# Kernel tuning notes

Measured on AMD Instinct MI355X. Metric: run time of the kernel, lower is better.

## Reference

```python
import jax, jax.numpy as jnp
import numpy as np

N, E = 25000, 400000
ATOM, INV, DNODE, DEDGE = 64, 64, 128, 128
HID = 6 * INV  # invariance_net hidden = 4*inv + 2*inv


def _shift(x):
    # out[:-1] = x[1:]; out[-1] = 0  (matches torch zeros_like + slice assign)
    return jnp.concatenate([x[1:], jnp.zeros_like(x[:1])], axis=0)


def _ln(x, g, b):
    m = jnp.mean(x, axis=-1, keepdims=True)
    v = jnp.var(x, axis=-1, keepdims=True)
    return (x - m) * jax.lax.rsqrt(v + 1e-6) * g + b


def _block(x, w1, b1, g, bb, w2, b2):
    # Linear -> LayerNorm -> SiLU -> Linear
    h = jax.nn.silu(_ln(x @ w1.T + b1, g, bb))
    return h @ w2.T + b2


def _linear_params(key, din, dout):
    k1, k2 = jax.random.split(key)
    lim = 1.0 / np.sqrt(din)
    w = jax.random.uniform(k1, (dout, din), minval=-lim, maxval=lim, dtype=jnp.float32)
    b = jax.random.uniform(k2, (dout,), minval=-lim, maxval=lim, dtype=jnp.float32)
    return w, b


def setup_inputs():
    key = jax.random.key(0)
    ks = jax.random.split(key, 12)
    atom_embedded = jax.random.normal(ks[0], (N, ATOM), jnp.float32)
    edge_length_embedded = jax.random.normal(ks[1], (E, INV), jnp.float32)
    edge_vec = jax.random.normal(ks[2], (E, 3), jnp.float32)
    src = jnp.sort(jax.random.randint(ks[3], (E,), 0, N))  # neighbor-list layout
    dst = jax.random.randint(ks[4], (E,), 0, N)
    edge_index = jnp.stack([src, dst])
    aw1, ab1 = _linear_params(ks[5], 1, INV)
    aw2, ab2 = _linear_params(ks[6], INV, INV)
    iw1, ib1 = _linear_params(ks[7], 3 * INV + 3 * ATOM, HID)
    iw2, ib2 = _linear_params(ks[8], HID, DNODE)
    mw1, mb1 = _linear_params(ks[9], 2 * DNODE + INV, 2 * INV)
    mw2, mb2 = _linear_params(ks[10], 2 * INV, DEDGE)
    return dict(
        atom_embedded=atom_embedded, edge_length_embedded=edge_length_embedded,
        edge_vec=edge_vec, edge_index=edge_index,
        angle_w1=aw1, angle_b1=ab1, angle_g=jnp.ones(INV), angle_bn=jnp.zeros(INV),
        angle_w2=aw2, angle_b2=ab2,
        inv_w1=iw1, inv_b1=ib1, inv_g=jnp.ones(HID), inv_bn=jnp.zeros(HID),
        inv_w2=iw2, inv_b2=ib2,
        mrg_w1=mw1, mrg_b1=mb1, mrg_g=jnp.ones(2 * INV), mrg_bn=jnp.zeros(2 * INV),
        mrg_w2=mw2, mrg_b2=mb2,
    )


def _forward(atom_embedded, edge_length_embedded, edge_vec, edge_index,
             angle_w1, angle_b1, angle_g, angle_bn, angle_w2, angle_b2,
             inv_w1, inv_b1, inv_g, inv_bn, inv_w2, inv_b2,
             mrg_w1, mrg_b1, mrg_g, mrg_bn, mrg_w2, mrg_b2):
    src, dst = edge_index[0], edge_index[1]
    src_s, dst_s = _shift(src), _shift(dst)
    mask = (src == src_s) & (src != dst) & (src_s != dst_s)
    e = src.shape[0]
    ar = jnp.arange(e)
    # torch does nonzero(mask)[:-1]: drop the LAST true index from the mask
    last = jnp.max(jnp.where(mask, ar, -1))
    mask = mask & (ar != last)
    vn = edge_vec / jnp.linalg.norm(edge_vec, axis=-1, keepdims=True)
    vn = jnp.where(mask[:, None], vn, 0.0)  # edge_vec_norm (zeros off-mask)
    cos = jnp.sum(vn * _shift(vn), axis=-1, keepdims=True)  # [E,1]
    ang = _block(cos, angle_w1, angle_b1, angle_g, angle_bn, angle_w2, angle_b2)
    el_s = _shift(edge_length_embedded)
    feat = jnp.concatenate([atom_embedded[src], atom_embedded[dst], edge_length_embedded,
                            atom_embedded[dst_s], el_s, ang], axis=-1)  # [E, 3*INV+3*ATOM]
    feat = jnp.where(mask[:, None], feat, 0.0)
    node_msg = _block(feat, inv_w1, inv_b1, inv_g, inv_bn, inv_w2, inv_b2)  # [E, DNODE]
    node = jax.ops.segment_sum(node_msg, dst, num_segments=atom_embedded.shape[0])
    edge = _block(jnp.concatenate([node[src], node[dst], edge_length_embedded], axis=-1),
                  mrg_w1, mrg_b1, mrg_g, mrg_bn, mrg_w2, mrg_b2)  # [E, DEDGE]
    return node, edge


def reference(atom_embedded, edge_length_embedded, edge_vec, edge_index,
              angle_w1, angle_b1, angle_g, angle_bn, angle_w2, angle_b2,
              inv_w1, inv_b1, inv_g, inv_bn, inv_w2, inv_b2,
              mrg_w1, mrg_b1, mrg_g, mrg_bn, mrg_w2, mrg_b2):
    return _forward(atom_embedded, edge_length_embedded, edge_vec, edge_index,
                    angle_w1, angle_b1, angle_g, angle_bn, angle_w2, angle_b2,
                    inv_w1, inv_b1, inv_g, inv_bn, inv_w2, inv_b2,
                    mrg_w1, mrg_b1, mrg_g, mrg_bn, mrg_w2, mrg_b2)
```

## Files before the change

kernel.cpp:

```cpp
#include <hip/hip_runtime.h>
#include <math.h>


typedef short short8 __attribute__((ext_vector_type(8)));
typedef float f32x4 __attribute__((ext_vector_type(4)));

#define SFA 392
#define SFB 328

__device__ __forceinline__ unsigned short f2bf(float x) {
  union { float f; unsigned u; } v; v.f = x;
  unsigned r = (v.u + 0x7FFFu + ((v.u >> 16) & 1u)) >> 16;
  return (unsigned short)r;
}
__device__ __forceinline__ float bf2f(unsigned short h) {
  union { unsigned u; float f; } v; v.u = ((unsigned)h) << 16;
  return v.f;
}
__device__ __forceinline__ float silu_f(float x) { return x / (1.0f + __expf(-x)); }

__global__ void k_init(float* __restrict__ node_out, int n, int* __restrict__ last_idx) {
  int i = blockIdx.x * blockDim.x + threadIdx.x;
  if (i == 0) *last_idx = -1;
  for (; i < n; i += gridDim.x * blockDim.x) node_out[i] = 0.0f;
}

__global__ void k_mask(const int* __restrict__ src, const int* __restrict__ dst,
                       int E, unsigned char* __restrict__ rawmask, int* __restrict__ last_idx) {
  int i = blockIdx.x * blockDim.x + threadIdx.x;
  if (i >= E) return;
  int s0 = src[i], d0 = dst[i];
  int s1 = (i + 1 < E) ? src[i + 1] : 0;
  int d1 = (i + 1 < E) ? dst[i + 1] : 0;
  int m = (s0 == s1) && (s0 != d0) && (s1 != d1);
  rawmask[i] = (unsigned char)m;
  if (m) atomicMax(last_idx, i);
}

__global__ void k_setup(const float* __restrict__ iw1, const float* __restrict__ aw2,
                        const float* __restrict__ ab2,
                        const float* __restrict__ aw1, const float* __restrict__ ab1,
                        const float* __restrict__ ag,
                        float* __restrict__ Wfa, float* __restrict__ cfa,
                        float* __restrict__ wg, float* __restrict__ bg,
                        float* __restrict__ angp) {
  int n = blockIdx.x * blockDim.x + threadIdx.x;
  if (n < 384 * 64) {
    int r = n >> 6, j = n & 63;
    float acc = 0.0f;
    for (int k = 0; k < 64; ++k) acc += iw1[r * 384 + 320 + k] * aw2[k * 64 + j];
    Wfa[n] = acc;
  } else if (n < 384 * 64 + 384) {
    int r = n - 384 * 64;
    float acc = 0.0f;
    for (int k = 0; k < 64; ++k) acc += iw1[r * 384 + 320 + k] * ab2[k];
    cfa[r] = acc;
  } else if (n < 384 * 64 + 384 + 64) {
    int j = n - (384 * 64 + 384);
    float wm = 0.f, bm = 0.f;
    for (int k = 0; k < 64; ++k) { wm += aw1[k]; bm += ab1[k]; }
    wm *= (1.f / 64.f); bm *= (1.f / 64.f);
    wg[j] = (aw1[j] - wm) * ag[j];
    bg[j] = (ab1[j] - bm) * ag[j];
    if (j == 0) {
      float vw = 0.f, cwb = 0.f, vb = 0.f;
      for (int k = 0; k < 64; ++k) {
        float dw = aw1[k] - wm, db = ab1[k] - bm;
        vw += dw * dw; cwb += dw * db; vb += db * db;
      }
      angp[0] = vw * (1.f / 64.f);
      angp[1] = cwb * (1.f / 64.f);
      angp[2] = vb * (1.f / 64.f);
    }
  }
}

__global__ void k_swz(const float* __restrict__ iw1, const float* __restrict__ iw2,
                      const float* __restrict__ mw1, const float* __restrict__ mw2,
                      const float* __restrict__ Wfa,
                      unsigned short* __restrict__ B1, unsigned short* __restrict__ B2,
                      unsigned short* __restrict__ B3, unsigned short* __restrict__ B4) {
  const int NC1 = 24 * 12 * 64, NC2 = 8 * 12 * 64, NC3 = 8 * 10 * 64, NC4 = 8 * 4 * 64;
  int cid = blockIdx.x * blockDim.x + threadIdx.x;
  int region, rel, KT;
  unsigned short* out;
  if (cid < NC1)                    { region = 1; rel = cid;                KT = 12; out = B1; }
  else if (cid < NC1 + NC2)         { region = 2; rel = cid - NC1;          KT = 12; out = B2; }
  else if (cid < NC1 + NC2 + NC3)   { region = 3; rel = cid - NC1 - NC2;    KT = 10; out = B3; }
  else if (cid < NC1 + NC2 + NC3 + NC4) { region = 4; rel = cid - NC1 - NC2 - NC3; KT = 4; out = B4; }
  else return;
  int l = rel & 63;
  int ktn = rel >> 6;
  int kt = ktn % KT, nt = ktn / KT;
  int n = nt * 16 + (l & 15);
  int k0 = kt * 32 + ((l >> 4) & 3) * 8;
  short8 pk;
  #pragma unroll
  for (int j = 0; j < 8; ++j) {
    int k = k0 + j;
    float v;
    if (region == 1)      v = (k < 320) ? iw1[n * 384 + k] : Wfa[n * 64 + (k - 320)];
    else if (region == 2) v = iw2[n * 384 + k];
    else if (region == 3) v = mw1[n * 320 + k];
    else                  v = mw2[n * 128 + k];
    pk[j] = (short)f2bf(v);
  }
  *(short8*)(out + ((size_t)rel << 3)) = pk;
}

__global__ __launch_bounds__(256, 3)
void k_inv(const float* __restrict__ atom, const float* __restrict__ el,
           const float* __restrict__ ev,
           const int* __restrict__ src, const int* __restrict__ dst,
           const unsigned char* __restrict__ rawmask, const int* __restrict__ last_idx,
           const float* __restrict__ ib1, const float* __restrict__ ig,
           const float* __restrict__ ibn, const float* __restrict__ ib2,
           const float* __restrict__ cfa, const float* __restrict__ wg,
           const float* __restrict__ bg, const float* __restrict__ abn,
           const float* __restrict__ angp,
           const unsigned short* __restrict__ Bsw1, const unsigned short* __restrict__ Bsw2,
           float* __restrict__ node_out, int E) {
  __shared__ __attribute__((aligned(16))) unsigned short sf[64 * SFA];
  __shared__ float scos[64], srr[64], smaskf[64], smean[64], srstd[64];
  __shared__ int ssrc[64], sdst[64], sdsts[64];

  const int t = threadIdx.x;
  const int lane = t & 63;
  const int q = (lane >> 4) & 3;
  const int col = lane & 15;
  const int mbase = (t >> 6) * 16;
  const int geb = blockIdx.x * 64;

  if (t < 64) {
    int e = t, ge = geb + e;
    int last = *last_idx;
    int ok = ge < E;
    int m0 = 0, m1 = 0, s0 = 0, d0 = 0, d1 = 0;
    if (ok) { s0 = src[ge]; d0 = dst[ge]; m0 = rawmask[ge] && (ge != last); }
    if (ge + 1 < E) { d1 = dst[ge + 1]; m1 = rawmask[ge + 1] && (ge + 1 != last); }
    ssrc[e] = s0; sdst[e] = d0; sdsts[e] = d1;
    smaskf[e] = m0 ? 1.0f : 0.0f;
    float cosv = 0.f;
    if (m0 && m1) {
      float ax = ev[3 * ge], ay = ev[3 * ge + 1], az = ev[3 * ge + 2];
      float bx = ev[3 * ge + 3], by = ev[3 * ge + 4], bz = ev[3 * ge + 5];
      cosv = (ax * bx + ay * by + az * bz) *
             rsqrtf((ax * ax + ay * ay + az * az) * (bx * bx + by * by + bz * bz));
    }
    scos[e] = cosv;
    srr[e] = rsqrtf(cosv * cosv * angp[0] + 2.f * cosv * angp[1] + angp[2] + 1e-6f);
  }
  __syncthreads();

  {
    const int es = t >> 2, sub = t & 3;
    const int ge = geb + es;
    const float mk = smaskf[es];
    unsigned short* drw = sf + es * SFA;
    if (mk > 0.f) {
      const float* p0 = atom + (size_t)ssrc[es] * 64 + sub * 8;
      const float* p1 = atom + (size_t)sdst[es] * 64 + sub * 8;
      const float* p2 = el + (size_t)ge * 64 + sub * 8;
      const float* p3 = atom + (size_t)sdsts[es] * 64 + sub * 8;
      const float* p4 = el + (size_t)(ge + 1) * 64 + sub * 8;
      auto stage8 = [&](int colb, const float* sp) {
        float4 a = *(const float4*)sp;
        float4 b = *(const float4*)(sp + 4);
        short8 pk;
        pk[0] = (short)f2bf(a.x); pk[1] = (short)f2bf(a.y);
        pk[2] = (short)f2bf(a.z); pk[3] = (short)f2bf(a.w);
        pk[4] = (short)f2bf(b.x); pk[5] = (short)f2bf(b.y);
        pk[6] = (short)f2bf(b.z); pk[7] = (short)f2bf(b.w);
        *(short8*)(drw + colb) = pk;
      };
      stage8(sub * 8,        p0);  stage8(32 + sub * 8,  p0 + 32);
      stage8(64 + sub * 8,   p1);  stage8(96 + sub * 8,  p1 + 32);
      stage8(128 + sub * 8,  p2);  stage8(160 + sub * 8, p2 + 32);
      stage8(192 + sub * 8,  p3);  stage8(224 + sub * 8, p3 + 32);
      stage8(256 + sub * 8,  p4);  stage8(288 + sub * 8, p4 + 32);
      const float cosv = scos[es], rr = srr[es];
      #pragma unroll
      for (int ii = 0; ii < 2; ++ii) {
        const int j0 = sub * 8 + ii * 32;
        float4 w0 = *(const float4*)(wg + j0),  w1 = *(const float4*)(wg + j0 + 4);
        float4 g0 = *(const float4*)(bg + j0),  g1 = *(const float4*)(bg + j0 + 4);
        float4 n0 = *(const float4*)(abn + j0), n1 = *(const float4*)(abn + j0 + 4);
        short8 pk;
        pk[0] = (short)f2bf(silu_f((cosv * w0.x + g0.x) * rr + n0.x));
        pk[1] = (short)f2bf(silu_f((cosv * w0.y + g0.y) * rr + n0.y));
        pk[2] = (short)f2bf(silu_f((cosv * w0.z + g0.z) * rr + n0.z));
        pk[3] = (short)f2bf(silu_f((cosv * w0.w + g0.w) * rr + n0.w));
        pk[4] = (short)f2bf(silu_f((cosv * w1.x + g1.x) * rr + n1.x));
        pk[5] = (short)f2bf(silu_f((cosv * w1.y + g1.y) * rr + n1.y));
        pk[6] = (short)f2bf(silu_f((cosv * w1.z + g1.z) * rr + n1.z));
        pk[7] = (short)f2bf(silu_f((cosv * w1.w + g1.w) * rr + n1.w));
        *(short8*)(drw + 320 + j0) = pk;
      }
    } else {
      short8 z = {0, 0, 0, 0, 0, 0, 0, 0};
      #pragma unroll
      for (int ii = 0; ii < 12; ++ii)
        *(short8*)(drw + sub * 8 + ii * 32) = z;
    }
  }
  __syncthreads();

  short8 af[12];
  #pragma unroll
  for (int kt = 0; kt < 12; ++kt)
    af[kt] = *(const short8*)(sf + (mbase + col) * SFA + kt * 32 + q * 8);

  float mrow[4]; int drow[4];
  #pragma unroll
  for (int r = 0; r < 4; ++r) {
    int e = mbase + q * 4 + r;
    mrow[r] = smaskf[e];
    drow[r] = sdst[e];
  }

  float sums[4] = {0, 0, 0, 0}, sqs[4] = {0, 0, 0, 0};
  {
    short8 bfA[12], bfB[12];
    #pragma unroll
    for (int kt = 0; kt < 12; ++kt)
      bfA[kt] = *(const short8*)(Bsw1 + (((0 * 12 + kt) * 64 + lane) << 3));
    #pragma unroll 1
    for (int ntp = 0; ntp < 12; ++ntp) {
      const int nt0 = 2 * ntp, nt1 = nt0 + 1;
      const bool pf = (ntp < 11);
      {
        int n = nt0 * 16 + col;
        float biasv = ib1[n], cfav = cfa[n];
        f32x4 acc;
        #pragma unroll
        for (int r = 0; r < 4; ++r) acc[r] = biasv + mrow[r] * cfav;
        #pragma unroll
        for (int kt = 0; kt < 12; ++kt) {
          bfB[kt] = *(const short8*)(Bsw1 + (((nt1 * 12 + kt) * 64 + lane) << 3));
          acc = __builtin_amdgcn_mfma_f32_16x16x32_bf16(af[kt], bfA[kt], acc, 0, 0, 0);
        }
        #pragma unroll
        for (int r = 0; r < 4; ++r) {
          float vv = acc[r];
          sums[r] += vv; sqs[r] += vv * vv;
          sf[(mbase + q * 4 + r) * SFA + nt0 * 16 + col] = f2bf(vv);
        }
      }
      {
        int n = nt1 * 16 + col;
        float biasv = ib1[n], cfav = cfa[n];
        f32x4 acc;
        #pragma unroll
        for (int r = 0; r < 4; ++r) acc[r] = biasv + mrow[r] * cfav;
        #pragma unroll
        for (int kt = 0; kt < 12; ++kt) {
          if (pf)
            bfA[kt] = *(const short8*)(Bsw1 + ((((nt0 + 2) * 12 + kt) * 64 + lane) << 3));
          acc = __builtin_amdgcn_mfma_f32_16x16x32_bf16(af[kt], bfB[kt], acc, 0, 0, 0);
        }
        #pragma unroll
        for (int r = 0; r < 4; ++r) {
          float vv = acc[r];
          sums[r] += vv; sqs[r] += vv * vv;
          sf[(mbase + q * 4 + r) * SFA + nt1 * 16 + col] = f2bf(vv);
        }
      }
    }
  }

  #pragma unroll
  for (int r = 0; r < 4; ++r) {
    float s = sums[r], ss = sqs[r];
    for (int m = 1; m < 16; m <<= 1) { s += __shfl_xor(s, m, 64); ss += __shfl_xor(ss, m, 64); }
    sums[r] = s; sqs[r] = ss;
  }
  if (col == 0) {
    #pragma unroll
    for (int r = 0; r < 4; ++r) {
      float mean = sums[r] * (1.f / 384.f);
      float var = sqs[r] * (1.f / 384.f) - mean * mean;
      smean[mbase + q * 4 + r] = mean;
      srstd[mbase + q * 4 + r] = rsqrtf(var + 1e-6f);
    }
  }
  __syncthreads();

  short8 af2[12];
  {
    int e = mbase + col;
    float mean = smean[e], rstd = srstd[e];
    #pragma unroll
    for (int kt = 0; kt < 12; ++kt) {
      int kb = kt * 32 + q * 8;
      short8 h8 = *(const short8*)(sf + e * SFA + kb);
      float4 g0 = *(const float4*)(ig + kb),  g1 = *(const float4*)(ig + kb + 4);
      float4 b0 = *(const float4*)(ibn + kb), b1v = *(const float4*)(ibn + kb + 4);
      float G[8] = {g0.x, g0.y, g0.z, g0.w, g1.x, g1.y, g1.z, g1.w};
      float B[8] = {b0.x, b0.y, b0.z, b0.w, b1v.x, b1v.y, b1v.z, b1v.w};
      short8 pk;
      #pragma unroll
      for (int j = 0; j < 8; ++j) {
        float h = bf2f((unsigned short)h8[j]);
        float hn = (h - mean) * rstd * G[j] + B[j];
        pk[j] = (short)f2bf(silu_f(hn));
      }
      af2[kt] = pk;
    }
  }
  {
    short8 bfA[12], bfB[12];
    #pragma unroll
    for (int kt = 0; kt < 12; ++kt)
      bfA[kt] = *(const short8*)(Bsw2 + (((0 * 12 + kt) * 64 + lane) << 3));
    #pragma unroll 1
    for (int ntp = 0; ntp < 4; ++ntp) {
      const int nt0 = 2 * ntp, nt1 = nt0 + 1;
      const bool pf = (ntp < 3);
      {
        int n = nt0 * 16 + col;
        float biasv = ib2[n];
        f32x4 acc;
        #pragma unroll
        for (int r = 0; r < 4; ++r) acc[r] = biasv;
        #pragma unroll
        for (int kt = 0; kt < 12; ++kt) {
          bfB[kt] = *(const short8*)(Bsw2 + (((nt1 * 12 + kt) * 64 + lane) << 3));
          acc = __builtin_amdgcn_mfma_f32_16x16x32_bf16(af2[kt], bfA[kt], acc, 0, 0, 0);
        }
        #pragma unroll
        for (int r = 0; r < 4; ++r) {
          int ge = geb + mbase + q * 4 + r;
          if (ge < E) atomicAdd(node_out + (size_t)drow[r] * 128 + n, acc[r]);
        }
      }
      {
        int n = nt1 * 16 + col;
        float biasv = ib2[n];
        f32x4 acc;
        #pragma unroll
        for (int r = 0; r < 4; ++r) acc[r] = biasv;
        #pragma unroll
        for (int kt = 0; kt < 12; ++kt) {
          if (pf)
            bfA[kt] = *(const short8*)(Bsw2 + ((((nt0 + 2) * 12 + kt) * 64 + lane) << 3));
          acc = __builtin_amdgcn_mfma_f32_16x16x32_bf16(af2[kt], bfB[kt], acc, 0, 0, 0);
        }
        #pragma unroll
        for (int r = 0; r < 4; ++r) {
          int ge = geb + mbase + q * 4 + r;
          if (ge < E) atomicAdd(node_out + (size_t)drow[r] * 128 + n, acc[r]);
        }
      }
    }
  }
}

__global__ __launch_bounds__(256, 3)
void k_mrg(const float* __restrict__ node, const float* __restrict__ el,
           const int* __restrict__ src, const int* __restrict__ dst,
           const float* __restrict__ mb1, const float* __restrict__ mg,
           const float* __restrict__ mbn, const float* __restrict__ mb2,
           const unsigned short* __restrict__ Bsw3, const unsigned short* __restrict__ Bsw4,
           float* __restrict__ edge_out, int E) {
  __shared__ __attribute__((aligned(16))) unsigned short sf[64 * SFB];
  __shared__ float smean[64], srstd[64];
  __shared__ int ssrc[64], sdst[64];

  const int t = threadIdx.x;
  const int lane = t & 63;
  const int q = (lane >> 4) & 3;
  const int col = lane & 15;
  const int mbase = (t >> 6) * 16;
  const int geb = blockIdx.x * 64;

  if (t < 64) {
    int ge = geb + t;
    int ok = ge < E;
    ssrc[t] = ok ? src[ge] : 0;
    sdst[t] = ok ? dst[ge] : 0;
  }
  __syncthreads();

  {
    const int es = t >> 2, sub = t & 3;
    const int ge = geb + es;
    unsigned short* drw = sf + es * SFB;
    if (ge < E) {
      const float* p0 = node + (size_t)ssrc[es] * 128 + sub * 8;
      const float* p1 = node + (size_t)sdst[es] * 128 + sub * 8;
      const float* p2 = el + (size_t)ge * 64 + sub * 8;
      auto stage8 = [&](int colb, const float* sp) {
        float4 a = *(const float4*)sp;
        float4 b = *(const float4*)(sp + 4);
        short8 pk;
        pk[0] = (short)f2bf(a.x); pk[1] = (short)f2bf(a.y);
        pk[2] = (short)f2bf(a.z); pk[3] = (short)f2bf(a.w);
        pk[4] = (short)f2bf(b.x); pk[5] = (short)f2bf(b.y);
        pk[6] = (short)f2bf(b.z); pk[7] = (short)f2bf(b.w);
        *(short8*)(drw + colb) = pk;
      };
      stage8(sub * 8,        p0);       stage8(32 + sub * 8,  p0 + 32);
      stage8(64 + sub * 8,   p0 + 64);  stage8(96 + sub * 8,  p0 + 96);
      stage8(128 + sub * 8,  p1);       stage8(160 + sub * 8, p1 + 32);
      stage8(192 + sub * 8,  p1 + 64);  stage8(224 + sub * 8, p1 + 96);
      stage8(256 + sub * 8,  p2);       stage8(288 + sub * 8, p2 + 32);
    } else {
      short8 z = {0, 0, 0, 0, 0, 0, 0, 0};
      #pragma unroll
      for (int ii = 0; ii < 10; ++ii)
        *(short8*)(drw + sub * 8 + ii * 32) = z;
    }
  }
  __syncthreads();

  short8 af[10];
  #pragma unroll
  for (int kt = 0; kt < 10; ++kt)
    af[kt] = *(const short8*)(sf + (mbase + col) * SFB + kt * 32 + q * 8);

  float sums[4] = {0, 0, 0, 0}, sqs[4] = {0, 0, 0, 0};
  {
    short8 bfA[10], bfB[10];
    #pragma unroll
    for (int kt = 0; kt < 10; ++kt)
      bfA[kt] = *(const short8*)(Bsw3 + (((0 * 10 + kt) * 64 + lane) << 3));
    #pragma unroll 1
    for (int ntp = 0; ntp < 4; ++ntp) {
      const int nt0 = 2 * ntp, nt1 = nt0 + 1;
      const bool pf = (ntp < 3);
      {
        int n = nt0 * 16 + col;
        float biasv = mb1[n];
        f32x4 acc;
        #pragma unroll
        for (int r = 0; r < 4; ++r) acc[r] = biasv;
        #pragma unroll
        for (int kt = 0; kt < 10; ++kt) {
          bfB[kt] = *(const short8*)(Bsw3 + (((nt1 * 10 + kt) * 64 + lane) << 3));
          acc = __builtin_amdgcn_mfma_f32_16x16x32_bf16(af[kt], bfA[kt], acc, 0, 0, 0);
        }
        #pragma unroll
        for (int r = 0; r < 4; ++r) {
          float vv = acc[r];
          sums[r] += vv; sqs[r] += vv * vv;
          sf[(mbase + q * 4 + r) * SFB + nt0 * 16 + col] = f2bf(vv);
        }
      }
      {
        int n = nt1 * 16 + col;
        float biasv = mb1[n];
        f32x4 acc;
        #pragma unroll
        for (int r = 0; r < 4; ++r) acc[r] = biasv;
        #pragma unroll
        for (int kt = 0; kt < 10; ++kt) {
          if (pf)
            bfA[kt] = *(const short8*)(Bsw3 + ((((nt0 + 2) * 10 + kt) * 64 + lane) << 3));
          acc = __builtin_amdgcn_mfma_f32_16x16x32_bf16(af[kt], bfB[kt], acc, 0, 0, 0);
        }
        #pragma unroll
        for (int r = 0; r < 4; ++r) {
          float vv = acc[r];
          sums[r] += vv; sqs[r] += vv * vv;
          sf[(mbase + q * 4 + r) * SFB + nt1 * 16 + col] = f2bf(vv);
        }
      }
    }
  }

  #pragma unroll
  for (int r = 0; r < 4; ++r) {
    float s = sums[r], ss = sqs[r];
    for (int m = 1; m < 16; m <<= 1) { s += __shfl_xor(s, m, 64); ss += __shfl_xor(ss, m, 64); }
    sums[r] = s; sqs[r] = ss;
  }
  if (col == 0) {
    #pragma unroll
    for (int r = 0; r < 4; ++r) {
      float mean = sums[r] * (1.f / 128.f);
      float var = sqs[r] * (1.f / 128.f) - mean * mean;
      smean[mbase + q * 4 + r] = mean;
      srstd[mbase + q * 4 + r] = rsqrtf(var + 1e-6f);
    }
  }
  __syncthreads();

  short8 af2[4];
  {
    int e = mbase + col;
    float mean = smean[e], rstd = srstd[e];
    #pragma unroll
    for (int kt = 0; kt < 4; ++kt) {
      int kb = kt * 32 + q * 8;
      short8 h8 = *(const short8*)(sf + e * SFB + kb);
      float4 g0 = *(const float4*)(mg + kb),  g1 = *(const float4*)(mg + kb + 4);
      float4 b0 = *(const float4*)(mbn + kb), b1v = *(const float4*)(mbn + kb + 4);
      float G[8] = {g0.x, g0.y, g0.z, g0.w, g1.x, g1.y, g1.z, g1.w};
      float B[8] = {b0.x, b0.y, b0.z, b0.w, b1v.x, b1v.y, b1v.z, b1v.w};
      short8 pk;
      #pragma unroll
      for (int j = 0; j < 8; ++j) {
        float h = bf2f((unsigned short)h8[j]);
        float hn = (h - mean) * rstd * G[j] + B[j];
        pk[j] = (short)f2bf(silu_f(hn));
      }
      af2[kt] = pk;
    }
  }
  {
    short8 bfA[4], bfB[4];
    #pragma unroll
    for (int kt = 0; kt < 4; ++kt)
      bfA[kt] = *(const short8*)(Bsw4 + (((0 * 4 + kt) * 64 + lane) << 3));
    #pragma unroll 1
    for (int ntp = 0; ntp < 4; ++ntp) {
      const int nt0 = 2 * ntp, nt1 = nt0 + 1;
      const bool pf = (ntp < 3);
      {
        int n = nt0 * 16 + col;
        float biasv = mb2[n];
        f32x4 acc;
        #pragma unroll
        for (int r = 0; r < 4; ++r) acc[r] = biasv;
        #pragma unroll
        for (int kt = 0; kt < 4; ++kt) {
          bfB[kt] = *(const short8*)(Bsw4 + (((nt1 * 4 + kt) * 64 + lane) << 3));
          acc = __builtin_amdgcn_mfma_f32_16x16x32_bf16(af2[kt], bfA[kt], acc, 0, 0, 0);
        }
        #pragma unroll
        for (int r = 0; r < 4; ++r) {
          int ge = geb + mbase + q * 4 + r;
          if (ge < E) edge_out[(size_t)ge * 128 + n] = acc[r];
        }
      }
      {
        int n = nt1 * 16 + col;
        float biasv = mb2[n];
        f32x4 acc;
        #pragma unroll
        for (int r = 0; r < 4; ++r) acc[r] = biasv;
        #pragma unroll
        for (int kt = 0; kt < 4; ++kt) {
          if (pf)
            bfA[kt] = *(const short8*)(Bsw4 + ((((nt0 + 2) * 4 + kt) * 64 + lane) << 3));
          acc = __builtin_amdgcn_mfma_f32_16x16x32_bf16(af2[kt], bfB[kt], acc, 0, 0, 0);
        }
        #pragma unroll
        for (int r = 0; r < 4; ++r) {
          int ge = geb + mbase + q * 4 + r;
          if (ge < E) edge_out[(size_t)ge * 128 + n] = acc[r];
        }
      }
    }
  }
}

extern "C" void kernel_launch(void* const* d_in, const int* in_sizes, int n_in,
                              void* d_out, int out_size, void* d_ws, size_t ws_size,
                              hipStream_t stream) {
  const float* atom = (const float*)d_in[0];
  const float* el   = (const float*)d_in[1];
  const float* ev   = (const float*)d_in[2];
  const int*   eidx = (const int*)d_in[3];
  const float* aw1  = (const float*)d_in[4];
  const float* ab1  = (const float*)d_in[5];
  const float* ag   = (const float*)d_in[6];
  const float* abn  = (const float*)d_in[7];
  const float* aw2  = (const float*)d_in[8];
  const float* ab2  = (const float*)d_in[9];
  const float* iw1  = (const float*)d_in[10];
  const float* ib1  = (const float*)d_in[11];
  const float* ig   = (const float*)d_in[12];
  const float* ibn  = (const float*)d_in[13];
  const float* iw2  = (const float*)d_in[14];
  const float* ib2  = (const float*)d_in[15];
  const float* mw1  = (const float*)d_in[16];
  const float* mb1  = (const float*)d_in[17];
  const float* mg   = (const float*)d_in[18];
  const float* mbn  = (const float*)d_in[19];
  const float* mw2  = (const float*)d_in[20];
  const float* mb2  = (const float*)d_in[21];

  const int N = in_sizes[0] / 64;
  const int E = in_sizes[1] / 64;
  const int* src = eidx;
  const int* dst = eidx + E;

  char* ws = (char*)d_ws;
  size_t off = 0;
  int* last_idx = (int*)(ws + off);          off += 256;
  unsigned char* rawmask = (unsigned char*)(ws + off); off += ((size_t)E + 255) & ~(size_t)255;
  float* Wfa  = (float*)(ws + off);          off += (size_t)384 * 64 * 4;
  float* cfa  = (float*)(ws + off);          off += 384 * 4;
  float* wg   = (float*)(ws + off);          off += 256;
  float* bg   = (float*)(ws + off);          off += 256;
  float* angp = (float*)(ws + off);          off += 256;
  unsigned short* B1 = (unsigned short*)(ws + off); off += (size_t)24 * 12 * 64 * 8 * 2;
  unsigned short* B2 = (unsigned short*)(ws + off); off += (size_t)8 * 12 * 64 * 8 * 2;
  unsigned short* B3 = (unsigned short*)(ws + off); off += (size_t)8 * 10 * 64 * 8 * 2;
  unsigned short* B4 = (unsigned short*)(ws + off); off += (size_t)8 * 4 * 64 * 8 * 2;

  float* node_out = (float*)d_out;
  float* edge_out = node_out + (size_t)N * 128;

  const int eb = (E + 255) / 256;
  const int tb = (E + 63) / 64;
  const int swz_n = 24 * 12 * 64 + 8 * 12 * 64 + 8 * 10 * 64 + 8 * 4 * 64;

  k_init<<<2048, 256, 0, stream>>>(node_out, N * 128, last_idx);
  k_mask<<<eb, 256, 0, stream>>>(src, dst, E, rawmask, last_idx);
  k_setup<<<(384 * 64 + 384 + 64 + 255) / 256, 256, 0, stream>>>(
      iw1, aw2, ab2, aw1, ab1, ag, Wfa, cfa, wg, bg, angp);
  k_swz<<<(swz_n + 255) / 256, 256, 0, stream>>>(iw1, iw2, mw1, mw2, Wfa, B1, B2, B3, B4);
  k_inv<<<tb, 256, 0, stream>>>(atom, el, ev, src, dst, rawmask, last_idx,
                                ib1, ig, ibn, ib2, cfa, wg, bg, abn, angp,
                                B1, B2, node_out, E);
  k_mrg<<<tb, 256, 0, stream>>>(node_out, el, src, dst,
                                mb1, mg, mbn, mb2, B3, B4, edge_out, E);
}
```

Measured before the change: 1.171 ms.

## Stage weight fragments cooperatively through double-buffered LDS instead of per-wave global loads

Each of the four waves used to load every pre-swizzled bf16 weight fragment from global or L2 on its own. Now the waves split each 16-column weight tile between them, write it into a double-buffered LDS area and sync before the MFMAs read it. This cuts global load traffic per block by about four times and frees the large bfA/bfB register arrays. In exchange it adds a __syncthreads per half or full tile and extra LDS use, and launch bounds drop from 3 to 2 blocks per SM.

After: 1.020 ms. -12.8%, faster.

```diff
diff --git a/kernel.cpp b/kernel.cpp
--- a/kernel.cpp
+++ b/kernel.cpp
@@ -108,7 +108,7 @@
   *(short8*)(out + ((size_t)rel << 3)) = pk;
 }
 
-__global__ __launch_bounds__(256, 3)
+__global__ __launch_bounds__(256, 2)
 void k_inv(const float* __restrict__ atom, const float* __restrict__ el,
            const float* __restrict__ ev,
            const int* __restrict__ src, const int* __restrict__ dst,
@@ -121,15 +121,30 @@
            const unsigned short* __restrict__ Bsw1, const unsigned short* __restrict__ Bsw2,
            float* __restrict__ node_out, int E) {
   __shared__ __attribute__((aligned(16))) unsigned short sf[64 * SFA];
+  __shared__ __attribute__((aligned(16))) unsigned short wb0[6 * 512];
+  __shared__ __attribute__((aligned(16))) unsigned short wb1[6 * 512];
   __shared__ float scos[64], srr[64], smaskf[64], smean[64], srstd[64];
   __shared__ int ssrc[64], sdst[64], sdsts[64];
 
   const int t = threadIdx.x;
   const int lane = t & 63;
+  const int w = t >> 6;
   const int q = (lane >> 4) & 3;
   const int col = lane & 15;
-  const int mbase = (t >> 6) * 16;
+  const int mbase = w * 16;
   const int geb = blockIdx.x * 64;
+
+  short8 stgA, stgB;
+  auto issue6 = [&](const unsigned short* B, int fb) {
+    stgA = *(const short8*)(B + (((size_t)(fb + w) * 64 + lane) << 3));
+    if (w < 2) stgB = *(const short8*)(B + (((size_t)(fb + 4 + w) * 64 + lane) << 3));
+  };
+  auto write6 = [&](unsigned short* wb) {
+    *(short8*)(wb + w * 512 + lane * 8) = stgA;
+    if (w < 2) *(short8*)(wb + (w + 4) * 512 + lane * 8) = stgB;
+  };
+
+  issue6(Bsw1, 0);
 
   if (t < 64) {
     int e = t, ge = geb + e;
@@ -203,6 +218,7 @@
         *(short8*)(drw + sub * 8 + ii * 32) = z;
     }
   }
+  write6(wb0);
   __syncthreads();
 
   short8 af[12];
@@ -219,53 +235,36 @@
   }
 
   float sums[4] = {0, 0, 0, 0}, sqs[4] = {0, 0, 0, 0};
-  {
-    short8 bfA[12], bfB[12];
-    #pragma unroll
-    for (int kt = 0; kt < 12; ++kt)
-      bfA[kt] = *(const short8*)(Bsw1 + (((0 * 12 + kt) * 64 + lane) << 3));
-    #pragma unroll 1
-    for (int ntp = 0; ntp < 12; ++ntp) {
-      const int nt0 = 2 * ntp, nt1 = nt0 + 1;
-      const bool pf = (ntp < 11);
-      {
-        int n = nt0 * 16 + col;
-        float biasv = ib1[n], cfav = cfa[n];
-        f32x4 acc;
-        #pragma unroll
-        for (int r = 0; r < 4; ++r) acc[r] = biasv + mrow[r] * cfav;
-        #pragma unroll
-        for (int kt = 0; kt < 12; ++kt) {
-          bfB[kt] = *(const short8*)(Bsw1 + (((nt1 * 12 + kt) * 64 + lane) << 3));
-          acc = __builtin_amdgcn_mfma_f32_16x16x32_bf16(af[kt], bfA[kt], acc, 0, 0, 0);
-        }
-        #pragma unroll
-        for (int r = 0; r < 4; ++r) {
-          float vv = acc[r];
-          sums[r] += vv; sqs[r] += vv * vv;
-          sf[(mbase + q * 4 + r) * SFA + nt0 * 16 + col] = f2bf(vv);
-        }
-      }
-      {
-        int n = nt1 * 16 + col;
-        float biasv = ib1[n], cfav = cfa[n];
-        f32x4 acc;
-        #pragma unroll
-        for (int r = 0; r < 4; ++r) acc[r] = biasv + mrow[r] * cfav;
-        #pragma unroll
-        for (int kt = 0; kt < 12; ++kt) {
-          if (pf)
-            bfA[kt] = *(const short8*)(Bsw1 + ((((nt0 + 2) * 12 + kt) * 64 + lane) << 3));
-          acc = __builtin_amdgcn_mfma_f32_16x16x32_bf16(af[kt], bfB[kt], acc, 0, 0, 0);
-        }
-        #pragma unroll
-        for (int r = 0; r < 4; ++r) {
-          float vv = acc[r];
-          sums[r] += vv; sqs[r] += vv * vv;
-          sf[(mbase + q * 4 + r) * SFA + nt1 * 16 + col] = f2bf(vv);
-        }
-      }
-    }
+  float bv = ib1[col], cv = cfa[col];
+  #pragma unroll 1
+  for (int nt = 0; nt < 24; ++nt) {
+    issue6(Bsw1, nt * 12 + 6);
+    f32x4 acc;
+    #pragma unroll
+    for (int r = 0; r < 4; ++r) acc[r] = bv + mrow[r] * cv;
+    #pragma unroll
+    for (int kt = 0; kt < 6; ++kt) {
+      short8 bw = *(const short8*)(wb0 + kt * 512 + lane * 8);
+      acc = __builtin_amdgcn_mfma_f32_16x16x32_bf16(af[kt], bw, acc, 0, 0, 0);
+    }
+    write6(wb1);
+    __syncthreads();
+    if (nt < 23) issue6(Bsw1, (nt + 1) * 12);
+    else         issue6(Bsw2, 0);
+    #pragma unroll
+    for (int kt = 0; kt < 6; ++kt) {
+      short8 bw = *(const short8*)(wb1 + kt * 512 + lane * 8);
+      acc = __builtin_amdgcn_mfma_f32_16x16x32_bf16(af[6 + kt], bw, acc, 0, 0, 0);
+    }
+    if (nt < 23) { bv = ib1[(nt + 1) * 16 + col]; cv = cfa[(nt + 1) * 16 + col]; }
+    #pragma unroll
+    for (int r = 0; r < 4; ++r) {
+      float vv = acc[r];
+      sums[r] += vv; sqs[r] += vv * vv;
+      sf[(mbase + q * 4 + r) * SFA + nt * 16 + col] = f2bf(vv);
+    }
+    write6(wb0);
+    __syncthreads();
   }
 
   #pragma unroll
@@ -307,55 +306,38 @@
       af2[kt] = pk;
     }
   }
-  {
-    short8 bfA[12], bfB[12];
-    #pragma unroll
-    for (int kt = 0; kt < 12; ++kt)
-      bfA[kt] = *(const short8*)(Bsw2 + (((0 * 12 + kt) * 64 + lane) << 3));
-    #pragma unroll 1
-    for (int ntp = 0; ntp < 4; ++ntp) {
-      const int nt0 = 2 * ntp, nt1 = nt0 + 1;
-      const bool pf = (ntp < 3);
-      {
-        int n = nt0 * 16 + col;
-        float biasv = ib2[n];
-        f32x4 acc;
-        #pragma unroll
-        for (int r = 0; r < 4; ++r) acc[r] = biasv;
-        #pragma unroll
-        for (int kt = 0; kt < 12; ++kt) {
-          bfB[kt] = *(const short8*)(Bsw2 + (((nt1 * 12 + kt) * 64 + lane) << 3));
-          acc = __builtin_amdgcn_mfma_f32_16x16x32_bf16(af2[kt], bfA[kt], acc, 0, 0, 0);
-        }
-        #pragma unroll
-        for (int r = 0; r < 4; ++r) {
-          int ge = geb + mbase + q * 4 + r;
-          if (ge < E) atomicAdd(node_out + (size_t)drow[r] * 128 + n, acc[r]);
-        }
-      }
-      {
-        int n = nt1 * 16 + col;
-        float biasv = ib2[n];
-        f32x4 acc;
-        #pragma unroll
-        for (int r = 0; r < 4; ++r) acc[r] = biasv;
-        #pragma unroll
-        for (int kt = 0; kt < 12; ++kt) {
-          if (pf)
-            bfA[kt] = *(const short8*)(Bsw2 + ((((nt0 + 2) * 12 + kt) * 64 + lane) << 3));
-          acc = __builtin_amdgcn_mfma_f32_16x16x32_bf16(af2[kt], bfB[kt], acc, 0, 0, 0);
-        }
-        #pragma unroll
-        for (int r = 0; r < 4; ++r) {
-          int ge = geb + mbase + q * 4 + r;
-          if (ge < E) atomicAdd(node_out + (size_t)drow[r] * 128 + n, acc[r]);
-        }
-      }
-    }
-  }
-}
-
-__global__ __launch_bounds__(256, 3)
+
+  float bv2 = ib2[col];
+  #pragma unroll 1
+  for (int nt = 0; nt < 8; ++nt) {
+    issue6(Bsw2, nt * 12 + 6);
+    f32x4 acc;
+    #pragma unroll
+    for (int r = 0; r < 4; ++r) acc[r] = bv2;
+    #pragma unroll
+    for (int kt = 0; kt < 6; ++kt) {
+      short8 bw = *(const short8*)(wb0 + kt * 512 + lane * 8);
+      acc = __builtin_amdgcn_mfma_f32_16x16x32_bf16(af2[kt], bw, acc, 0, 0, 0);
+    }
+    write6(wb1);
+    __syncthreads();
+    if (nt < 7) issue6(Bsw2, (nt + 1) * 12);
+    #pragma unroll
+    for (int kt = 0; kt < 6; ++kt) {
+      short8 bw = *(const short8*)(wb1 + kt * 512 + lane * 8);
+      acc = __builtin_amdgcn_mfma_f32_16x16x32_bf16(af2[6 + kt], bw, acc, 0, 0, 0);
+    }
+    if (nt < 7) bv2 = ib2[(nt + 1) * 16 + col];
+    #pragma unroll
+    for (int r = 0; r < 4; ++r) {
+      int ge = geb + mbase + q * 4 + r;
+      if (ge < E) atomicAdd(node_out + (size_t)drow[r] * 128 + (nt * 16 + col), acc[r]);
+    }
+    if (nt < 7) { write6(wb0); __syncthreads(); }
+  }
+}
+
+__global__ __launch_bounds__(256, 2)
 void k_mrg(const float* __restrict__ node, const float* __restrict__ el,
            const int* __restrict__ src, const int* __restrict__ dst,
            const float* __restrict__ mb1, const float* __restrict__ mg,
@@ -363,15 +345,38 @@
            const unsigned short* __restrict__ Bsw3, const unsigned short* __restrict__ Bsw4,
            float* __restrict__ edge_out, int E) {
   __shared__ __attribute__((aligned(16))) unsigned short sf[64 * SFB];
+  __shared__ __attribute__((aligned(16))) unsigned short wbA[10 * 512];
+  __shared__ __attribute__((aligned(16))) unsigned short wbB[10 * 512];
   __shared__ float smean[64], srstd[64];
   __shared__ int ssrc[64], sdst[64];
 
   const int t = threadIdx.x;
   const int lane = t & 63;
+  const int w = t >> 6;
   const int q = (lane >> 4) & 3;
   const int col = lane & 15;
-  const int mbase = (t >> 6) * 16;
+  const int mbase = w * 16;
   const int geb = blockIdx.x * 64;
+
+  short8 stgA, stgB, stgC;
+  auto issue10 = [&](const unsigned short* B, int fb) {
+    stgA = *(const short8*)(B + (((size_t)(fb + w) * 64 + lane) << 3));
+    stgB = *(const short8*)(B + (((size_t)(fb + 4 + w) * 64 + lane) << 3));
+    if (w < 2) stgC = *(const short8*)(B + (((size_t)(fb + 8 + w) * 64 + lane) << 3));
+  };
+  auto write10 = [&](unsigned short* wb) {
+    *(short8*)(wb + w * 512 + lane * 8) = stgA;
+    *(short8*)(wb + (w + 4) * 512 + lane * 8) = stgB;
+    if (w < 2) *(short8*)(wb + (w + 8) * 512 + lane * 8) = stgC;
+  };
+  auto issue4 = [&](const unsigned short* B, int fb) {
+    stgA = *(const short8*)(B + (((size_t)(fb + w) * 64 + lane) << 3));
+  };
+  auto write4 = [&](unsigned short* wb) {
+    *(short8*)(wb + w * 512 + lane * 8) = stgA;
+  };
+
+  issue10(Bsw3, 0);
 
   if (t < 64) {
     int ge = geb + t;
@@ -411,6 +416,7 @@
         *(short8*)(drw + sub * 8 + ii * 32) = z;
     }
   }
+  write10(wbA);
   __syncthreads();
 
   short8 af[10];
@@ -419,53 +425,30 @@
     af[kt] = *(const short8*)(sf + (mbase + col) * SFB + kt * 32 + q * 8);
 
   float sums[4] = {0, 0, 0, 0}, sqs[4] = {0, 0, 0, 0};
-  {
-    short8 bfA[10], bfB[10];
-    #pragma unroll
-    for (int kt = 0; kt < 10; ++kt)
-      bfA[kt] = *(const short8*)(Bsw3 + (((0 * 10 + kt) * 64 + lane) << 3));
-    #pragma unroll 1
-    for (int ntp = 0; ntp < 4; ++ntp) {
-      const int nt0 = 2 * ntp, nt1 = nt0 + 1;
-      const bool pf = (ntp < 3);
-      {
-        int n = nt0 * 16 + col;
-        float biasv = mb1[n];
-        f32x4 acc;
-        #pragma unroll
-        for (int r = 0; r < 4; ++r) acc[r] = biasv;
-        #pragma unroll
-        for (int kt = 0; kt < 10; ++kt) {
-          bfB[kt] = *(const short8*)(Bsw3 + (((nt1 * 10 + kt) * 64 + lane) << 3));
-          acc = __builtin_amdgcn_mfma_f32_16x16x32_bf16(af[kt], bfA[kt], acc, 0, 0, 0);
-        }
-        #pragma unroll
-        for (int r = 0; r < 4; ++r) {
-          float vv = acc[r];
-          sums[r] += vv; sqs[r] += vv * vv;
-          sf[(mbase + q * 4 + r) * SFB + nt0 * 16 + col] = f2bf(vv);
-        }
-      }
-      {
-        int n = nt1 * 16 + col;
-        float biasv = mb1[n];
-        f32x4 acc;
-        #pragma unroll
-        for (int r = 0; r < 4; ++r) acc[r] = biasv;
-        #pragma unroll
-        for (int kt = 0; kt < 10; ++kt) {
-          if (pf)
-            bfA[kt] = *(const short8*)(Bsw3 + ((((nt0 + 2) * 10 + kt) * 64 + lane) << 3));
-          acc = __builtin_amdgcn_mfma_f32_16x16x32_bf16(af[kt], bfB[kt], acc, 0, 0, 0);
-        }
-        #pragma unroll
-        for (int r = 0; r < 4; ++r) {
-          float vv = acc[r];
-          sums[r] += vv; sqs[r] += vv * vv;
-          sf[(mbase + q * 4 + r) * SFB + nt1 * 16 + col] = f2bf(vv);
-        }
-      }
-    }
+  float bv = mb1[col];
+  #pragma unroll 1
+  for (int nt = 0; nt < 8; ++nt) {
+    unsigned short* rb = (nt & 1) ? wbB : wbA;
+    unsigned short* sb = (nt & 1) ? wbA : wbB;
+    if (nt < 7) issue10(Bsw3, (nt + 1) * 10);
+    else        issue4(Bsw4, 0);
+    f32x4 acc;
+    #pragma unroll
+    for (int r = 0; r < 4; ++r) acc[r] = bv;
+    #pragma unroll
+    for (int kt = 0; kt < 10; ++kt) {
+      short8 bw = *(const short8*)(rb + kt * 512 + lane * 8);
+      acc = __builtin_amdgcn_mfma_f32_16x16x32_bf16(af[kt], bw, acc, 0, 0, 0);
+    }
+    if (nt < 7) bv = mb1[(nt + 1) * 16 + col];
+    #pragma unroll
+    for (int r = 0; r < 4; ++r) {
+      float vv = acc[r];
+      sums[r] += vv; sqs[r] += vv * vv;
+      sf[(mbase + q * 4 + r) * SFB + nt * 16 + col] = f2bf(vv);
+    }
+    if (nt < 7) write10(sb); else write4(sb);
+    __syncthreads();
   }
 
   #pragma unroll
@@ -507,51 +490,28 @@
       af2[kt] = pk;
     }
   }
-  {
-    short8 bfA[4], bfB[4];
-    #pragma unroll
-    for (int kt = 0; kt < 4; ++kt)
-      bfA[kt] = *(const short8*)(Bsw4 + (((0 * 4 + kt) * 64 + lane) << 3));
-    #pragma unroll 1
-    for (int ntp = 0; ntp < 4; ++ntp) {
-      const int nt0 = 2 * ntp, nt1 = nt0 + 1;
-      const bool pf = (ntp < 3);
-      {
-        int n = nt0 * 16 + col;
-        float biasv = mb2[n];
-        f32x4 acc;
-        #pragma unroll
-        for (int r = 0; r < 4; ++r) acc[r] = biasv;
-        #pragma unroll
-        for (int kt = 0; kt < 4; ++kt) {
-          bfB[kt] = *(const short8*)(Bsw4 + (((nt1 * 4 + kt) * 64 + lane) << 3));
-          acc = __builtin_amdgcn_mfma_f32_16x16x32_bf16(af2[kt], bfA[kt], acc, 0, 0, 0);
-        }
-        #pragma unroll
-        for (int r = 0; r < 4; ++r) {
-          int ge = geb + mbase + q * 4 + r;
-          if (ge < E) edge_out[(size_t)ge * 128 + n] = acc[r];
-        }
-      }
-      {
-        int n = nt1 * 16 + col;
-        float biasv = mb2[n];
-        f32x4 acc;
-        #pragma unroll
-        for (int r = 0; r < 4; ++r) acc[r] = biasv;
-        #pragma unroll
-        for (int kt = 0; kt < 4; ++kt) {
-          if (pf)
-            bfA[kt] = *(const short8*)(Bsw4 + ((((nt0 + 2) * 4 + kt) * 64 + lane) << 3));
-          acc = __builtin_amdgcn_mfma_f32_16x16x32_bf16(af2[kt], bfB[kt], acc, 0, 0, 0);
-        }
-        #pragma unroll
-        for (int r = 0; r < 4; ++r) {
-          int ge = geb + mbase + q * 4 + r;
-          if (ge < E) edge_out[(size_t)ge * 128 + n] = acc[r];
-        }
-      }
-    }
+
+  float bv2 = mb2[col];
+  #pragma unroll 1
+  for (int nt = 0; nt < 8; ++nt) {
+    unsigned short* rb = (nt & 1) ? wbB : wbA;
+    unsigned short* sb = (nt & 1) ? wbA : wbB;
+    if (nt < 7) issue4(Bsw4, (nt + 1) * 4);
+    f32x4 acc;
+    #pragma unroll
+    for (int r = 0; r < 4; ++r) acc[r] = bv2;
+    #pragma unroll
+    for (int kt = 0; kt < 4; ++kt) {
+      short8 bw = *(const short8*)(rb + kt * 512 + lane * 8);
+      acc = __builtin_amdgcn_mfma_f32_16x16x32_bf16(af2[kt], bw, acc, 0, 0, 0);
+    }
+    if (nt < 7) bv2 = mb2[(nt + 1) * 16 + col];
+    #pragma unroll
+    for (int r = 0; r < 4; ++r) {
+      int ge = geb + mbase + q * 4 + r;
+      if (ge < E) edge_out[(size_t)ge * 128 + (nt * 16 + col)] = acc[r];
+    }
+    if (nt < 7) { write4(sb); __syncthreads(); }
   }
 }
 
```
